# Performance work log

Hardware: AMD Instinct MI355X
Metric: run time of the kernel (lower is better)

Reference implementation:

```python
import jax, jax.numpy as jnp
import numpy as np

N_ENT = 14951   # entities (FB15K-style multimodal KG)
N_REL = 1345    # relations == number of context sub-graphs
N_NODES = 120000  # nodes in the batched context graph (b_x length)
N_EDGES = 480000  # edges in the normalized batched adjacency


def _glorot(key, shape):
    scale = np.sqrt(2.0 / (shape[0] + shape[1])).astype(np.float32)
    return jax.random.normal(key, shape, dtype=jnp.float32) * scale


def setup_inputs() -> dict:
    key = jax.random.key(0)
    ks = jax.random.split(key, 16)
    inp = {}
    inp["img_feat"] = jax.random.normal(ks[0], (N_ENT, 4096), dtype=jnp.float32)
    inp["text_feat"] = jax.random.normal(ks[1], (N_ENT, 300), dtype=jnp.float32)
    inp["rel_emb"] = jax.random.normal(ks[2], (N_REL, 300), dtype=jnp.float32)
    # learned parameters (eval mode: dropout = identity)
    inp["W_img_text"] = _glorot(ks[3], (4396, 100)); inp["b_img_text"] = jnp.zeros((100,), jnp.float32)
    inp["W_rel_input"] = _glorot(ks[4], (300, 100)); inp["b_rel_input"] = jnp.zeros((100,), jnp.float32)
    inp["W_gc1"] = _glorot(ks[5], (200, 256)); inp["b_gc1"] = jnp.zeros((256,), jnp.float32)
    inp["W_gc2"] = _glorot(ks[6], (256, 200)); inp["b_gc2"] = jnp.zeros((200,), jnp.float32)
    inp["W_emb"] = _glorot(ks[7], (400, 1)); inp["b_emb"] = jnp.zeros((1,), jnp.float32)
    inp["W_emb_out"] = _glorot(ks[8], (400, 200)); inp["b_emb_out"] = jnp.zeros((200,), jnp.float32)
    inp["W_rel"] = _glorot(ks[9], (300, 200)); inp["b_rel"] = jnp.zeros((200,), jnp.float32)
    # row-normalized adjacency of the batched context graph, as edge list
    inp["edge_weight"] = jax.random.uniform(ks[10], (N_EDGES,), dtype=jnp.float32)
    inp["b_x"] = jax.random.randint(ks[11], (N_NODES,), 0, N_ENT)
    inp["b_graph"] = jax.random.randint(ks[12], (N_NODES,), 0, N_REL)
    inp["edge_src"] = jax.random.randint(ks[13], (N_EDGES,), 0, N_NODES)
    inp["edge_dst"] = jax.random.randint(ks[14], (N_EDGES,), 0, N_NODES)
    return inp


def reference(img_feat, text_feat, rel_emb, W_img_text, b_img_text, W_rel_input,
              b_rel_input, W_gc1, b_gc1, W_gc2, b_gc2, W_emb, b_emb, W_emb_out,
              b_emb_out, W_rel, b_rel, edge_weight, b_x, b_graph, edge_src, edge_dst):
    seg_sum = lambda v, idx, n: jax.ops.segment_sum(v, idx, num_segments=n)

    def spmm(h):  # normalized adjacency @ h via edge-list gather/scatter
        return seg_sum(h[edge_src] * edge_weight[:, None], edge_dst, N_NODES)

    # multimodal entity encoder: Linear(4396 -> 100)
    emf = jnp.concatenate([img_feat, text_feat], axis=1) @ W_img_text + b_img_text
    # relation context encoder: Linear(300 -> 100) + ReLU
    rel_in = jax.nn.relu(rel_emb @ W_rel_input + b_rel_input)
    # batched context-graph node features [M, 200]
    h = jnp.concatenate([emf[b_x], rel_in[b_graph]], axis=1)
    # two-layer GCN encoder (SGCN1)
    h1 = jax.nn.relu(spmm(h @ W_gc1) + b_gc1)
    h2 = spmm(h1 @ W_gc2) + b_gc2          # [M, 200]
    # scatter_mean over entity ids, broadcast back
    cnt = seg_sum(jnp.ones((N_NODES,), h2.dtype), b_x, N_ENT)
    mean = seg_sum(h2, b_x, N_ENT) / jnp.maximum(cnt, 1.0)[:, None]
    emb = jnp.concatenate([h2, mean[b_x]], axis=1)   # [M, 400]
    score = emb @ W_emb + b_emb                      # [M, 1]
    # scatter_softmax over segments b_x (numerically stable)
    smax = jax.ops.segment_max(score, b_x, num_segments=N_ENT)
    e = jnp.exp(score - smax[b_x])
    z_s = e / seg_sum(e, b_x, N_ENT)[b_x]
    new_out = seg_sum(z_s * emb, b_x, N_ENT) @ W_emb_out + b_emb_out  # [N_ENT, 200]
    # relation output encoder: Linear(300 -> 200) + ReLU
    rel_context = jax.nn.relu(rel_emb @ W_rel + b_rel)                # [N_REL, 200]
    return new_out, rel_context
```

## Files before the change

### kernel.cpp

```cpp
#include <hip/hip_runtime.h>

#define N_ENT 14951
#define N_REL 1345
#define NNODE 120000
#define NEDGE 480000
#define MP_ENC 14976
#define KP_ENC 4480
#define NP_ENC 112
#define ENC_SPLIT 4
#define ENC_KSPLIT 1120
#define ENC_STEPS 35
#define MROWS1 16320
#define NB_E 118
#define NB_N 15

static inline int ceil_div(int a, int b){ return (a + b - 1) / b; }

typedef __bf16 bf16x8 __attribute__((ext_vector_type(8)));
typedef float f32x4 __attribute__((ext_vector_type(4)));

__device__ inline unsigned short f2bf(float f){
  unsigned u = __float_as_uint(f);
  return (unsigned short)((u + 0x7fffu + ((u >> 16) & 1u)) >> 16);
}
__device__ inline float bf2f(unsigned short b){
  return __uint_as_float(((unsigned)b) << 16);
}

__global__ __launch_bounds__(256) void enc_mfma(
    const float* __restrict__ img, const float* __restrict__ txt,
    const unsigned short* __restrict__ Wt1, float* __restrict__ part)
{
  __shared__ unsigned short As[64 * 40];
  __shared__ unsigned short Bs[112 * 40];
  const int t = threadIdx.x;
  const int m0 = blockIdx.x * 64;
  const int s = blockIdx.y;
  const int l = t & 63, w = t >> 6;
  f32x4 acc[7];
  #pragma unroll
  for (int i = 0; i < 7; i++) acc[i] = f32x4{0.f, 0.f, 0.f, 0.f};

  for (int step = 0; step < ENC_STEPS; ++step) {
    const int kb = s * ENC_KSPLIT + step * 32;
    #pragma unroll
    for (int p = 0; p < 2; ++p) {
      const int c = t + p * 256;
      const int row = c >> 3, kq = c & 7;
      const int rowg = m0 + row;
      const int k = kb + kq * 4;
      float4 v = make_float4(0.f, 0.f, 0.f, 0.f);
      if (rowg < N_ENT) {
        if (k < 4096)      v = *(const float4*)(img + (size_t)rowg * 4096 + k);
        else if (k < 4396) v = *(const float4*)(txt + (size_t)rowg * 300 + (k - 4096));
      }
      ushort4 b;
      b.x = f2bf(v.x); b.y = f2bf(v.y); b.z = f2bf(v.z); b.w = f2bf(v.w);
      *(ushort4*)&As[row * 40 + kq * 4] = b;
    }
    {
      const int n = t >> 2, k16 = t & 3;
      *(uint4*)&Bs[n * 40 + k16 * 8] = *(const uint4*)(Wt1 + (size_t)n * KP_ENC + kb + k16 * 8);
      if (t < 192) {
        const int c = t + 256;
        const int n2 = c >> 2, k2 = c & 3;
        *(uint4*)&Bs[n2 * 40 + k2 * 8] = *(const uint4*)(Wt1 + (size_t)n2 * KP_ENC + kb + k2 * 8);
      }
    }
    __syncthreads();
    bf16x8 a = *(const bf16x8*)&As[(w * 16 + (l & 15)) * 40 + (l >> 4) * 8];
    #pragma unroll
    for (int ct = 0; ct < 7; ++ct) {
      bf16x8 bb = *(const bf16x8*)&Bs[(ct * 16 + (l & 15)) * 40 + (l >> 4) * 8];
      acc[ct] = __builtin_amdgcn_mfma_f32_16x16x32_bf16(a, bb, acc[ct], 0, 0, 0);
    }
    __syncthreads();
  }
  const int rb = m0 + w * 16 + (l >> 4) * 4;
  const int col = l & 15;
  float* pp = part + (size_t)s * MP_ENC * NP_ENC;
  #pragma unroll
  for (int ct = 0; ct < 7; ++ct)
    #pragma unroll
    for (int i = 0; i < 4; ++i)
      pp[(size_t)(rb + i) * NP_ENC + ct * 16 + col] = acc[ct][i];
}

__global__ __launch_bounds__(256) void enc_reduce(
    const float* __restrict__ part, const float* __restrict__ bias,
    unsigned short* __restrict__ feat1)
{
  int i = blockIdx.x * 256 + threadIdx.x;
  if (i >= N_ENT * 100) return;
  int r = i / 100, c = i % 100;
  float v = bias[c];
  #pragma unroll
  for (int s = 0; s < ENC_SPLIT; ++s) v += part[((size_t)s * MP_ENC + r) * NP_ENC + c];
  feat1[(size_t)r * 224 + c] = f2bf(v);
}

__global__ __launch_bounds__(256) void rel_enc(
    const float* __restrict__ rel, const float* __restrict__ W_ri,
    const float* __restrict__ b_ri, unsigned short* __restrict__ feat1)
{
  __shared__ float rs[300];
  const int r = blockIdx.x;
  const int t = threadIdx.x;
  if (t < 75) {
    float4 v = *(const float4*)(rel + (size_t)r * 300 + t * 4);
    *(float4*)&rs[t * 4] = v;
  }
  __syncthreads();
  if (t >= 100) return;
  float s = b_ri[t];
  for (int k = 0; k < 300; ++k) s = fmaf(rs[k], W_ri[(size_t)k * 100 + t], s);
  feat1[(size_t)(N_ENT + r) * 224 + 100 + t] = f2bf(fmaxf(s, 0.f));
}

__global__ __launch_bounds__(256) void egr1_mfma(
    const unsigned short* __restrict__ feat1, const unsigned short* __restrict__ Wtg1,
    unsigned short* __restrict__ egr1)
{
  __shared__ unsigned short As[64 * 40];
  __shared__ unsigned short Bs[256 * 40];
  const int t = threadIdx.x;
  const int m0 = blockIdx.x * 64;
  const int l = t & 63, w = t >> 6;
  f32x4 acc[16];
  #pragma unroll
  for (int i = 0; i < 16; i++) acc[i] = f32x4{0.f, 0.f, 0.f, 0.f};

  for (int step = 0; step < 7; ++step) {
    const int kb = step * 32;
    {
      const int row = t >> 2, kc = t & 3;
      *(uint4*)&As[row * 40 + kc * 8] = *(const uint4*)(feat1 + (size_t)(m0 + row) * 224 + kb + kc * 8);
    }
    #pragma unroll
    for (int p = 0; p < 4; ++p) {
      const int c = t + p * 256;
      const int n = c >> 2, k16 = c & 3;
      *(uint4*)&Bs[n * 40 + k16 * 8] = *(const uint4*)(Wtg1 + (size_t)n * 224 + kb + k16 * 8);
    }
    __syncthreads();
    bf16x8 a = *(const bf16x8*)&As[(w * 16 + (l & 15)) * 40 + (l >> 4) * 8];
    #pragma unroll
    for (int ct = 0; ct < 16; ++ct) {
      bf16x8 bb = *(const bf16x8*)&Bs[(ct * 16 + (l & 15)) * 40 + (l >> 4) * 8];
      acc[ct] = __builtin_amdgcn_mfma_f32_16x16x32_bf16(a, bb, acc[ct], 0, 0, 0);
    }
    __syncthreads();
  }
  const int rb = m0 + w * 16 + (l >> 4) * 4;
  const int col0 = l & 15;
  #pragma unroll
  for (int ct = 0; ct < 16; ++ct) {
    const int col = ct * 16 + col0;
    #pragma unroll
    for (int i = 0; i < 4; ++i)
      egr1[(size_t)(rb + i) * 256 + col] = f2bf(acc[ct][i]);
  }
}

__global__ __launch_bounds__(256) void gemm2_mfma(
    const unsigned short* __restrict__ h1, const unsigned short* __restrict__ Wt2,
    unsigned short* __restrict__ hg2)
{
  __shared__ unsigned short As[64 * 40];
  __shared__ unsigned short Bs[208 * 40];
  const int t = threadIdx.x;
  const int m0 = blockIdx.x * 64;
  const int l = t & 63, w = t >> 6;
  f32x4 acc[13];
  #pragma unroll
  for (int i = 0; i < 13; i++) acc[i] = f32x4{0.f, 0.f, 0.f, 0.f};

  for (int step = 0; step < 8; ++step) {
    const int kb = step * 32;
    {
      const int row = t >> 2, kc = t & 3;
      *(uint4*)&As[row * 40 + kc * 8] = *(const uint4*)(h1 + (size_t)(m0 + row) * 256 + kb + kc * 8);
    }
    #pragma unroll
    for (int p = 0; p < 4; ++p) {
      const int c = t + p * 256;
      if (c < 832) {
        const int n = c >> 2, k16 = c & 3;
        *(uint4*)&Bs[n * 40 + k16 * 8] = *(const uint4*)(Wt2 + (size_t)n * 256 + kb + k16 * 8);
      }
    }
    __syncthreads();
    bf16x8 a = *(const bf16x8*)&As[(w * 16 + (l & 15)) * 40 + (l >> 4) * 8];
    #pragma unroll
    for (int ct = 0; ct < 13; ++ct) {
      bf16x8 bb = *(const bf16x8*)&Bs[(ct * 16 + (l & 15)) * 40 + (l >> 4) * 8];
      acc[ct] = __builtin_amdgcn_mfma_f32_16x16x32_bf16(a, bb, acc[ct], 0, 0, 0);
    }
    __syncthreads();
  }
  const int rb = m0 + w * 16 + (l >> 4) * 4;
  const int col0 = l & 15;
  #pragma unroll
  for (int ct = 0; ct < 13; ++ct) {
    const int col = ct * 16 + col0;
    #pragma unroll
    for (int i = 0; i < 4; ++i)
      hg2[(size_t)(rb + i) * 208 + col] = f2bf(acc[ct][i]);
  }
}

__global__ __launch_bounds__(256) void fin_mfma(
    const unsigned short* __restrict__ embA, const unsigned short* __restrict__ Wteo,
    const float* __restrict__ b_eo, float* __restrict__ out)
{
  __shared__ unsigned short As[64 * 40];
  __shared__ unsigned short Bs[208 * 40];
  const int t = threadIdx.x;
  const int m0 = blockIdx.x * 64;
  const int l = t & 63, w = t >> 6;
  f32x4 acc[13];
  #pragma unroll
  for (int i = 0; i < 13; i++) acc[i] = f32x4{0.f, 0.f, 0.f, 0.f};

  for (int step = 0; step < 13; ++step) {
    const int kb = step * 32;
    {
      const int row = t >> 2, kc = t & 3;
      *(uint4*)&As[row * 40 + kc * 8] = *(const uint4*)(embA + (size_t)(m0 + row) * 416 + kb + kc * 8);
    }
    #pragma unroll
    for (int p = 0; p < 4; ++p) {
      const int c = t + p * 256;
      if (c < 832) {
        const int n = c >> 2, k16 = c & 3;
        *(uint4*)&Bs[n * 40 + k16 * 8] = *(const uint4*)(Wteo + (size_t)n * 416 + kb + k16 * 8);
      }
    }
    __syncthreads();
    bf16x8 a = *(const bf16x8*)&As[(w * 16 + (l & 15)) * 40 + (l >> 4) * 8];
    #pragma unroll
    for (int ct = 0; ct < 13; ++ct) {
      bf16x8 bb = *(const bf16x8*)&Bs[(ct * 16 + (l & 15)) * 40 + (l >> 4) * 8];
      acc[ct] = __builtin_amdgcn_mfma_f32_16x16x32_bf16(a, bb, acc[ct], 0, 0, 0);
    }
    __syncthreads();
  }
  const int rb = m0 + w * 16 + (l >> 4) * 4;
  const int col0 = l & 15;
  #pragma unroll
  for (int ct = 0; ct < 13; ++ct) {
    const int col = ct * 16 + col0;
    if (col < 200) {
      const float b = b_eo[col];
      #pragma unroll
      for (int i = 0; i < 4; ++i) {
        const int r = rb + i;
        if (r < N_ENT) out[(size_t)r * 200 + col] = acc[ct][i] + b;
      }
    }
  }
}

__global__ __launch_bounds__(256) void wt_all_k(
    const float* __restrict__ W_it, const float* __restrict__ W_g1,
    const float* __restrict__ W_g2, const float* __restrict__ W_eo,
    unsigned short* __restrict__ Wt1, unsigned short* __restrict__ Wtg1,
    unsigned short* __restrict__ Wt2, unsigned short* __restrict__ Wteo)
{
  int i = blockIdx.x * 256 + threadIdx.x;
  if (i < NP_ENC * KP_ENC) {
    int n = i / KP_ENC, k = i % KP_ENC;
    float v = (n < 100 && k < 4396) ? W_it[(size_t)k * 100 + n] : 0.f;
    Wt1[i] = f2bf(v);
    return;
  }
  i -= NP_ENC * KP_ENC;
  if (i < 256 * 224) {
    int n = i / 224, k = i % 224;
    float v = (k < 200) ? W_g1[(size_t)k * 256 + n] : 0.f;
    Wtg1[i] = f2bf(v);
    return;
  }
  i -= 256 * 224;
  if (i < 208 * 256) {
    int n = i >> 8, k = i & 255;
    float v = (n < 200) ? W_g2[(size_t)k * 200 + n] : 0.f;
    Wt2[i] = f2bf(v);
    return;
  }
  i -= 208 * 256;
  if (i < 208 * 416) {
    int n = i / 416, k = i % 416;
    float v = (n < 200 && k < 400) ? W_eo[(size_t)k * 200 + n] : 0.f;
    Wteo[i] = f2bf(v);
  }
}

template<bool RELU, bool HASBIAS>
__global__ __launch_bounds__(256) void gemm_f32(
    const float* __restrict__ A1, int K1, const float* __restrict__ A2,
    const float* __restrict__ B, const float* __restrict__ bias,
    float* __restrict__ C, int M, int K, int N)
{
  constexpr int BM = 64, BN = 128, BK = 16;
  __shared__ float As[BK][BM + 4];
  __shared__ float Bs[BK][BN];
  const int t = threadIdx.x;
  const int m0 = blockIdx.y * BM, n0 = blockIdx.x * BN;
  const int tr = t >> 4, tc = t & 15;
  const int tm0 = tr * 4, tn0 = tc * 8;
  const int K2 = K - K1;
  const int arow = t >> 2, aq = (t & 3) * 4;
  const int brow = t >> 4, bc0 = (t & 15) * 4;
  float acc[4][8];
  #pragma unroll
  for (int i = 0; i < 4; i++)
    #pragma unroll
    for (int j = 0; j < 8; j++) acc[i][j] = 0.f;

  for (int k0 = 0; k0 < K; k0 += BK) {
    {
      const int r = m0 + arow;
      const int k = k0 + aq;
      float4 v = make_float4(0.f, 0.f, 0.f, 0.f);
      if (r < M) {
        if (k + 3 < K1) {
          v = *(const float4*)(A1 + (size_t)r * K1 + k);
        } else if (k >= K1 && (k - K1) + 3 < K2) {
          v = *(const float4*)(A2 + (size_t)r * K2 + (k - K1));
        } else {
          float tmp[4] = {0.f, 0.f, 0.f, 0.f};
          #pragma unroll
          for (int j = 0; j < 4; j++) {
            int kj = k + j;
            if (kj < K) tmp[j] = (kj < K1) ? A1[(size_t)r * K1 + kj]
                                           : A2[(size_t)r * K2 + (kj - K1)];
          }
          v = make_float4(tmp[0], tmp[1], tmp[2], tmp[3]);
        }
      }
      As[aq + 0][arow] = v.x; As[aq + 1][arow] = v.y;
      As[aq + 2][arow] = v.z; As[aq + 3][arow] = v.w;
    }
    {
      const int k = k0 + brow;
      #pragma unroll
      for (int h = 0; h < 2; h++) {
        const int n = n0 + bc0 + h * 64;
        float4 v = make_float4(0.f, 0.f, 0.f, 0.f);
        if (k < K) {
          if (n + 3 < N) {
            v = *(const float4*)(B + (size_t)k * N + n);
          } else {
            float tmp[4] = {0.f, 0.f, 0.f, 0.f};
            for (int j = 0; j < 4; j++) if (n + j < N) tmp[j] = B[(size_t)k * N + n + j];
            v = make_float4(tmp[0], tmp[1], tmp[2], tmp[3]);
          }
        }
        *(float4*)&Bs[brow][bc0 + h * 64] = v;
      }
    }
    __syncthreads();
    #pragma unroll
    for (int k = 0; k < BK; k++) {
      float a[4], b[8];
      *(float4*)&a[0] = *(const float4*)&As[k][tm0];
      *(float4*)&b[0] = *(const float4*)&Bs[k][tn0];
      *(float4*)&b[4] = *(const float4*)&Bs[k][tn0 + 4];
      #pragma unroll
      for (int i = 0; i < 4; i++)
        #pragma unroll
        for (int j = 0; j < 8; j++) acc[i][j] = fmaf(a[i], b[j], acc[i][j]);
    }
    __syncthreads();
  }
  #pragma unroll
  for (int i = 0; i < 4; i++) {
    const int r = m0 + tm0 + i;
    if (r >= M) continue;
    #pragma unroll
    for (int j = 0; j < 8; j++) {
      const int c = n0 + tn0 + j;
      if (c >= N) continue;
      float v = acc[i][j];
      if (HASBIAS) v += bias[c];
      if (RELU) v = fmaxf(v, 0.f);
      C[(size_t)r * N + c] = v;
    }
  }
}

__global__ __launch_bounds__(256) void hist2_k(
    const int* __restrict__ edst, const int* __restrict__ bx,
    int* __restrict__ ehist, int* __restrict__ nhist)
{
  int i = blockIdx.x * 256 + threadIdx.x;
  if (i < NEDGE) { atomicAdd(&ehist[edst[i]], 1); return; }
  i -= NEDGE;
  if (i < NNODE) atomicAdd(&nhist[bx[i]], 1);
}

__global__ __launch_bounds__(256) void scan1_k(
    const int* __restrict__ ehist, int* __restrict__ ebase, int* __restrict__ epart,
    const int* __restrict__ nhist, int* __restrict__ nbase, int* __restrict__ npart)
{
  __shared__ int s[256];
  const int t = threadIdx.x;
  const bool eregion = blockIdx.x < NB_E;
  const int b = eregion ? blockIdx.x : blockIdx.x - NB_E;
  const int n = eregion ? NNODE : N_ENT;
  const int* hist = eregion ? ehist : nhist;
  int* base = eregion ? ebase : nbase;
  int* partial = eregion ? epart : npart;
  const int i0 = b * 1024 + t * 4;
  int v[4];
  #pragma unroll
  for (int j = 0; j < 4; j++) v[j] = (i0 + j < n) ? hist[i0 + j] : 0;
  const int tsum = v[0] + v[1] + v[2] + v[3];
  s[t] = tsum;
  __syncthreads();
  #pragma unroll
  for (int off = 1; off < 256; off <<= 1) {
    int u = (t >= off) ? s[t - off] : 0;
    __syncthreads();
    s[t] += u;
    __syncthreads();
  }
  int run = s[t] - tsum;
  #pragma unroll
  for (int j = 0; j < 4; j++) {
    if (i0 + j < n) base[i0 + j] = run;
    run += v[j];
  }
  if (t == 255) partial[b] = s[255];
}

__global__ __launch_bounds__(256) void scan2_k(
    int* __restrict__ epart, int* __restrict__ ebase_end,
    int* __restrict__ npart, int* __restrict__ nbase_end)
{
  __shared__ int s[256];
  const int t = threadIdx.x;
  const bool eregion = blockIdx.x == 0;
  int* partial = eregion ? epart : npart;
  const int nb = eregion ? NB_E : NB_N;
  const int v = (t < nb) ? partial[t] : 0;
  s[t] = v;
  __syncthreads();
  #pragma unroll
  for (int off = 1; off < 256; off <<= 1) {
    int u = (t >= off) ? s[t - off] : 0;
    __syncthreads();
    s[t] += u;
    __syncthreads();
  }
  if (t < nb) partial[t] = s[t] - v;
  if (t == 255) *(eregion ? ebase_end : nbase_end) = s[255];
}

#define NB3_E 469
__global__ __launch_bounds__(256) void scan3_k(
    int* __restrict__ ebase, const int* __restrict__ epart,
    int* __restrict__ nbase, const int* __restrict__ npart)
{
  if (blockIdx.x < NB3_E) {
    int i = blockIdx.x * 256 + threadIdx.x;
    if (i < NNODE) ebase[i] += epart[i >> 10];
  } else {
    int i = (blockIdx.x - NB3_E) * 256 + threadIdx.x;
    if (i < N_ENT) nbase[i] += npart[i >> 10];
  }
}

__global__ __launch_bounds__(256) void scatter2_k(
    const int* __restrict__ esrc, const int* __restrict__ edst, const float* __restrict__ ew,
    const int* __restrict__ bx, const int* __restrict__ bg,
    const int* __restrict__ ebase, int* __restrict__ ecur,
    float* __restrict__ s_w, int* __restrict__ s_src,
    int* __restrict__ s_en, int* __restrict__ s_gn,
    const int* __restrict__ nbase, int* __restrict__ ncur, int* __restrict__ node_of)
{
  int i = blockIdx.x * 256 + threadIdx.x;
  if (i < NEDGE) {
    int d = edst[i];
    int p = ebase[d] + atomicAdd(&ecur[d], 1);
    int s = esrc[i];
    s_w[p] = ew[i];
    s_src[p] = s;
    s_en[p] = bx[s];
    s_gn[p] = bg[s];
    return;
  }
  i -= NEDGE;
  if (i < NNODE) {
    int ent = bx[i];
    int p = nbase[ent] + atomicAdd(&ncur[ent], 1);
    node_of[p] = i;
  }
}

__global__ __launch_bounds__(256) void spmm1_g(
    const int* __restrict__ ebase, const float* __restrict__ s_w,
    const int* __restrict__ s_en, const int* __restrict__ s_gn,
    const unsigned short* __restrict__ egr1,
    const float* __restrict__ b_g1, unsigned short* __restrict__ h1)
{
  const int gid = blockIdx.x * blockDim.x + threadIdx.x;
  const int d = gid >> 6, lane = gid & 63;
  if (d >= NNODE) return;
  const int p0 = ebase[d], p1 = ebase[d + 1];
  float acc[4] = {0.f, 0.f, 0.f, 0.f};
  for (int p = p0; p < p1; ++p) {
    const float w = s_w[p];
    const int en = s_en[p], gn = s_gn[p];
    const ushort4 va = *(const ushort4*)(egr1 + (size_t)en * 256 + lane * 4);
    const ushort4 vb = *(const ushort4*)(egr1 + (size_t)(N_ENT + gn) * 256 + lane * 4);
    acc[0] += w * (bf2f(va.x) + bf2f(vb.x));
    acc[1] += w * (bf2f(va.y) + bf2f(vb.y));
    acc[2] += w * (bf2f(va.z) + bf2f(vb.z));
    acc[3] += w * (bf2f(va.w) + bf2f(vb.w));
  }
  const float4 b = ((const float4*)b_g1)[lane];
  ushort4 o;
  o.x = f2bf(fmaxf(acc[0] + b.x, 0.f));
  o.y = f2bf(fmaxf(acc[1] + b.y, 0.f));
  o.z = f2bf(fmaxf(acc[2] + b.z, 0.f));
  o.w = f2bf(fmaxf(acc[3] + b.w, 0.f));
  *(ushort4*)(h1 + (size_t)d * 256 + lane * 4) = o;
}

__global__ __launch_bounds__(256) void spmm2_g(
    const int* __restrict__ ebase, const float* __restrict__ s_w,
    const int* __restrict__ s_src, const unsigned short* __restrict__ hg2,
    const float* __restrict__ b_g2, const float* __restrict__ W_e,
    unsigned short* __restrict__ h2, float* __restrict__ score)
{
  const int gid = blockIdx.x * blockDim.x + threadIdx.x;
  const int d = gid >> 6, lane = gid & 63;
  if (d >= NNODE) return;
  const int p0 = ebase[d], p1 = ebase[d + 1];
  float acc[4] = {0.f, 0.f, 0.f, 0.f};
  const int col = lane * 4;
  float sp = 0.f;
  if (lane < 50) {
    for (int p = p0; p < p1; ++p) {
      const float w = s_w[p];
      const ushort4 v = *(const ushort4*)(hg2 + (size_t)s_src[p] * 208 + col);
      acc[0] += w * bf2f(v.x); acc[1] += w * bf2f(v.y);
      acc[2] += w * bf2f(v.z); acc[3] += w * bf2f(v.w);
    }
    const float4 b = ((const float4*)b_g2)[lane];
    acc[0] += b.x; acc[1] += b.y; acc[2] += b.z; acc[3] += b.w;
    ushort4 o;
    o.x = f2bf(acc[0]); o.y = f2bf(acc[1]); o.z = f2bf(acc[2]); o.w = f2bf(acc[3]);
    *(ushort4*)(h2 + (size_t)d * 200 + col) = o;
    const float4 we = ((const float4*)W_e)[lane];
    sp = acc[0] * we.x + acc[1] * we.y + acc[2] * we.z + acc[3] * we.w;
  }
  #pragma unroll
  for (int off = 32; off; off >>= 1) sp += __shfl_xor(sp, off);
  if (lane == 0) score[d] = sp;
}

__global__ __launch_bounds__(256) void ent_k(
    const int* __restrict__ nbase, const int* __restrict__ node_of,
    const unsigned short* __restrict__ h2, const float* __restrict__ score,
    unsigned short* __restrict__ embA)
{
  const int gid = blockIdx.x * blockDim.x + threadIdx.x;
  const int ent = gid >> 6, lane = gid & 63;
  if (ent >= N_ENT) return;
  const int p0 = nbase[ent], p1 = nbase[ent + 1];
  const int cnt = p1 - p0;
  float m, es;
  if (cnt <= 64) {
    float sc = -3.4e38f;
    if (p0 + lane < p1) sc = score[node_of[p0 + lane]];
    m = sc;
    #pragma unroll
    for (int off = 32; off; off >>= 1) m = fmaxf(m, __shfl_xor(m, off));
    es = (p0 + lane < p1) ? __expf(sc - m) : 0.f;
    #pragma unroll
    for (int off = 32; off; off >>= 1) es += __shfl_xor(es, off);
  } else {
    m = -3.4e38f;
    for (int p = p0 + lane; p < p1; p += 64) m = fmaxf(m, score[node_of[p]]);
    #pragma unroll
    for (int off = 32; off; off >>= 1) m = fmaxf(m, __shfl_xor(m, off));
    es = 0.f;
    for (int p = p0 + lane; p < p1; p += 64) es += __expf(score[node_of[p]] - m);
    #pragma unroll
    for (int off = 32; off; off >>= 1) es += __shfl_xor(es, off);
  }
  const float inv_es = (cnt > 0) ? 1.f / es : 0.f;
  const float inv_cnt = 1.f / fmaxf((float)cnt, 1.f);
  float aw[4] = {0.f, 0.f, 0.f, 0.f};
  float am[4] = {0.f, 0.f, 0.f, 0.f};
  for (int p = p0; p < p1; ++p) {
    const int nd = node_of[p];
    const float z = __expf(score[nd] - m) * inv_es;
    if (lane < 50) {
      const ushort4 v = *(const ushort4*)(h2 + (size_t)nd * 200 + lane * 4);
      const float vx = bf2f(v.x), vy = bf2f(v.y), vz = bf2f(v.z), vw = bf2f(v.w);
      aw[0] += z * vx; aw[1] += z * vy; aw[2] += z * vz; aw[3] += z * vw;
      am[0] += vx; am[1] += vy; am[2] += vz; am[3] += vw;
    }
  }
  if (lane < 50) {
    ushort4 ow, om;
    ow.x = f2bf(aw[0]); ow.y = f2bf(aw[1]); ow.z = f2bf(aw[2]); ow.w = f2bf(aw[3]);
    om.x = f2bf(am[0] * inv_cnt); om.y = f2bf(am[1] * inv_cnt);
    om.z = f2bf(am[2] * inv_cnt); om.w = f2bf(am[3] * inv_cnt);
    *(ushort4*)(embA + (size_t)ent * 416 + lane * 4) = ow;
    *(ushort4*)(embA + (size_t)ent * 416 + 200 + lane * 4) = om;
  }
}

extern "C" void kernel_launch(void* const* d_in, const int* in_sizes, int n_in,
                              void* d_out, int out_size, void* d_ws, size_t ws_size,
                              hipStream_t stream)
{
  const float* img  = (const float*)d_in[0];
  const float* txt  = (const float*)d_in[1];
  const float* rel  = (const float*)d_in[2];
  const float* W_it = (const float*)d_in[3];
  const float* b_it = (const float*)d_in[4];
  const float* W_ri = (const float*)d_in[5];
  const float* b_ri = (const float*)d_in[6];
  const float* W_g1 = (const float*)d_in[7];
  const float* b_g1 = (const float*)d_in[8];
  const float* W_g2 = (const float*)d_in[9];
  const float* b_g2 = (const float*)d_in[10];
  const float* W_e  = (const float*)d_in[11];
  const float* W_eo = (const float*)d_in[13];
  const float* b_eo = (const float*)d_in[14];
  const float* W_r  = (const float*)d_in[15];
  const float* b_r  = (const float*)d_in[16];
  const float* ew   = (const float*)d_in[17];
  const int*   bx   = (const int*)d_in[18];
  const int*   bg   = (const int*)d_in[19];
  const int*   esrc = (const int*)d_in[20];
  const int*   edst = (const int*)d_in[21];

  float* ws = (float*)d_ws;
  size_t off = 0;
  auto alloc = [&](size_t n){ size_t r = off; off += (n + 255) & ~(size_t)255; return r; };
  unsigned short* feat1 = (unsigned short*)(ws + alloc((size_t)MROWS1 * 224 / 2));
  unsigned short* egr1  = (unsigned short*)(ws + alloc((size_t)MROWS1 * 256 / 2));
  unsigned short* h1    = (unsigned short*)(ws + alloc((size_t)NNODE * 256 / 2));
  unsigned short* hg2   = (unsigned short*)(ws + alloc((size_t)NNODE * 208 / 2));
  unsigned short* embA  = (unsigned short*)(ws + alloc((size_t)MP_ENC * 416 / 2));
  unsigned short* h2    = (unsigned short*)(ws + alloc((size_t)NNODE * 200 / 2));
  float* part  = ws + alloc((size_t)ENC_SPLIT * MP_ENC * NP_ENC);
  float* score = ws + alloc(NNODE);
  size_t cnt0 = alloc((size_t)NNODE * 2 + (size_t)N_ENT * 2);
  int* ehist = (int*)(ws + cnt0);
  int* ecur  = ehist + NNODE;
  int* nhist = ecur + NNODE;
  int* ncur  = nhist + N_ENT;
  int* ebase = (int*)(ws + alloc(NNODE + 1));
  int* nbase = (int*)(ws + alloc(N_ENT + 1));
  int* epart = (int*)(ws + alloc(256));
  int* npart = (int*)(ws + alloc(256));
  float* s_w  = ws + alloc(NEDGE);
  int* s_src  = (int*)(ws + alloc(NEDGE));
  int* s_en   = (int*)(ws + alloc(NEDGE));
  int* s_gn   = (int*)(ws + alloc(NEDGE));
  int* node_of = (int*)(ws + alloc(NNODE));
  unsigned short* Wt1  = (unsigned short*)(ws + alloc((size_t)NP_ENC * KP_ENC / 2));
  unsigned short* Wtg1 = (unsigned short*)(ws + alloc((size_t)256 * 224 / 2));
  unsigned short* Wt2  = (unsigned short*)(ws + alloc((size_t)208 * 256 / 2));
  unsigned short* Wteo = (unsigned short*)(ws + alloc((size_t)208 * 416 / 2));

  dim3 blk(256);

  hipMemsetAsync(ehist, 0, ((size_t)NNODE * 2 + (size_t)N_ENT * 2) * 4, stream);
  hipMemsetAsync(feat1, 0, (size_t)MROWS1 * 224 * 2, stream);
  hipMemsetAsync(embA,  0, (size_t)MP_ENC * 416 * 2, stream);

  hist2_k<<<ceil_div(NEDGE + NNODE, 256), blk, 0, stream>>>(edst, bx, ehist, nhist);
  scan1_k<<<NB_E + NB_N, blk, 0, stream>>>(ehist, ebase, epart, nhist, nbase, npart);
  scan2_k<<<2, blk, 0, stream>>>(epart, ebase + NNODE, npart, nbase + N_ENT);
  scan3_k<<<NB3_E + ceil_div(N_ENT, 256), blk, 0, stream>>>(ebase, epart, nbase, npart);
  scatter2_k<<<ceil_div(NEDGE + NNODE, 256), blk, 0, stream>>>(
      esrc, edst, ew, bx, bg, ebase, ecur, s_w, s_src, s_en, s_gn, nbase, ncur, node_of);

  wt_all_k<<<ceil_div(NP_ENC * KP_ENC + 256 * 224 + 208 * 256 + 208 * 416, 256), blk, 0, stream>>>(
      W_it, W_g1, W_g2, W_eo, Wt1, Wtg1, Wt2, Wteo);

  enc_mfma<<<dim3(MP_ENC / 64, ENC_SPLIT), blk, 0, stream>>>(img, txt, Wt1, part);
  enc_reduce<<<ceil_div(N_ENT * 100, 256), blk, 0, stream>>>(part, b_it, feat1);
  rel_enc<<<N_REL, blk, 0, stream>>>(rel, W_ri, b_ri, feat1);

  egr1_mfma<<<MROWS1 / 64, blk, 0, stream>>>(feat1, Wtg1, egr1);
  spmm1_g<<<ceil_div(NNODE * 64, 256), blk, 0, stream>>>(
      ebase, s_w, s_en, s_gn, egr1, b_g1, h1);

  gemm2_mfma<<<NNODE / 64, blk, 0, stream>>>(h1, Wt2, hg2);
  spmm2_g<<<ceil_div(NNODE * 64, 256), blk, 0, stream>>>(
      ebase, s_w, s_src, hg2, b_g2, W_e, h2, score);

  ent_k<<<ceil_div(N_ENT * 64, 256), blk, 0, stream>>>(nbase, node_of, h2, score, embA);

  float* out_new = (float*)d_out;
  float* out_rel = out_new + (size_t)N_ENT * 200;
  fin_mfma<<<MP_ENC / 64, blk, 0, stream>>>(embA, Wteo, b_eo, out_new);
  gemm_f32<true, true><<<dim3(2, ceil_div(N_REL, 64)), blk, 0, stream>>>(
      rel, 300, rel, W_r, b_r, out_rel, N_REL, 300, 200);
}
```

Before: 567.8 us.

## Widen encoder GEMM K-tile, raise split-K to 14, and reorder grid

The image/text encoder GEMM now stages a 64-wide K slice per step instead of 32, which halves the number of barrier pairs per unit of work. Split-K rises from 4 to 14 partitions, so far more blocks are available to fill the GPU. The grid is transposed so that neighbouring blocks cover different K ranges of the same 64 rows. The trade-off is a much larger partial-sum buffer that must be written and then read back by the reduction kernel, and it relies on that buffer and enc_reduce being sized from ENC_SPLIT.

```diff
diff --git a/kernel.cpp b/kernel.cpp
--- a/kernel.cpp
+++ b/kernel.cpp
@@ -7,9 +7,9 @@
 #define MP_ENC 14976
 #define KP_ENC 4480
 #define NP_ENC 112
-#define ENC_SPLIT 4
-#define ENC_KSPLIT 1120
-#define ENC_STEPS 35
+#define ENC_SPLIT 14
+#define ENC_KSPLIT 320
+#define ENC_STEPS 5
 #define MROWS1 16320
 #define NB_E 118
 #define NB_N 15
@@ -31,48 +31,60 @@
     const float* __restrict__ img, const float* __restrict__ txt,
     const unsigned short* __restrict__ Wt1, float* __restrict__ part)
 {
-  __shared__ unsigned short As[64 * 40];
-  __shared__ unsigned short Bs[112 * 40];
+  __shared__ unsigned short As[64 * 72];
+  __shared__ unsigned short Bs[112 * 72];
   const int t = threadIdx.x;
-  const int m0 = blockIdx.x * 64;
-  const int s = blockIdx.y;
+  const int s = blockIdx.x;
+  const int m0 = blockIdx.y * 64;
   const int l = t & 63, w = t >> 6;
   f32x4 acc[7];
   #pragma unroll
   for (int i = 0; i < 7; i++) acc[i] = f32x4{0.f, 0.f, 0.f, 0.f};
 
   for (int step = 0; step < ENC_STEPS; ++step) {
-    const int kb = s * ENC_KSPLIT + step * 32;
-    #pragma unroll
-    for (int p = 0; p < 2; ++p) {
-      const int c = t + p * 256;
-      const int row = c >> 3, kq = c & 7;
+    const int kb = s * ENC_KSPLIT + step * 64;
+    {
+      const int row = t >> 2;
+      const int q = (t & 3) * 16;
       const int rowg = m0 + row;
-      const int k = kb + kq * 4;
-      float4 v = make_float4(0.f, 0.f, 0.f, 0.f);
-      if (rowg < N_ENT) {
-        if (k < 4096)      v = *(const float4*)(img + (size_t)rowg * 4096 + k);
-        else if (k < 4396) v = *(const float4*)(txt + (size_t)rowg * 300 + (k - 4096));
+      const float* irow = img + (size_t)rowg * 4096;
+      const float* trow = txt + (size_t)rowg * 300;
+      ushort4 o[4];
+      #pragma unroll
+      for (int j = 0; j < 4; ++j) {
+        const int kj = kb + q + j * 4;
+        float4 v = make_float4(0.f, 0.f, 0.f, 0.f);
+        if (rowg < N_ENT) {
+          if (kj < 4096)       v = *(const float4*)(irow + kj);
+          else if (kj < 4396)  v = *(const float4*)(trow + (kj - 4096));
+        }
+        o[j].x = f2bf(v.x); o[j].y = f2bf(v.y); o[j].z = f2bf(v.z); o[j].w = f2bf(v.w);
       }
-      ushort4 b;
-      b.x = f2bf(v.x); b.y = f2bf(v.y); b.z = f2bf(v.z); b.w = f2bf(v.w);
-      *(ushort4*)&As[row * 40 + kq * 4] = b;
+      unsigned short* dst = &As[row * 72 + q];
+      *(ushort4*)(dst + 0)  = o[0];
+      *(ushort4*)(dst + 4)  = o[1];
+      *(ushort4*)(dst + 8)  = o[2];
+      *(ushort4*)(dst + 12) = o[3];
     }
     {
-      const int n = t >> 2, k16 = t & 3;
-      *(uint4*)&Bs[n * 40 + k16 * 8] = *(const uint4*)(Wt1 + (size_t)n * KP_ENC + kb + k16 * 8);
-      if (t < 192) {
-        const int c = t + 256;
-        const int n2 = c >> 2, k2 = c & 3;
-        *(uint4*)&Bs[n2 * 40 + k2 * 8] = *(const uint4*)(Wt1 + (size_t)n2 * KP_ENC + kb + k2 * 8);
+      #pragma unroll
+      for (int p = 0; p < 4; ++p) {
+        const int c = t + p * 256;
+        if (c < 896) {
+          const int n = c >> 3, ch = c & 7;
+          *(uint4*)&Bs[n * 72 + ch * 8] = *(const uint4*)(Wt1 + (size_t)n * KP_ENC + kb + ch * 8);
+        }
       }
     }
     __syncthreads();
-    bf16x8 a = *(const bf16x8*)&As[(w * 16 + (l & 15)) * 40 + (l >> 4) * 8];
-    #pragma unroll
-    for (int ct = 0; ct < 7; ++ct) {
-      bf16x8 bb = *(const bf16x8*)&Bs[(ct * 16 + (l & 15)) * 40 + (l >> 4) * 8];
-      acc[ct] = __builtin_amdgcn_mfma_f32_16x16x32_bf16(a, bb, acc[ct], 0, 0, 0);
+    #pragma unroll
+    for (int kh = 0; kh < 2; ++kh) {
+      bf16x8 a = *(const bf16x8*)&As[(w * 16 + (l & 15)) * 72 + kh * 32 + (l >> 4) * 8];
+      #pragma unroll
+      for (int ct = 0; ct < 7; ++ct) {
+        bf16x8 bb = *(const bf16x8*)&Bs[(ct * 16 + (l & 15)) * 72 + kh * 32 + (l >> 4) * 8];
+        acc[ct] = __builtin_amdgcn_mfma_f32_16x16x32_bf16(a, bb, acc[ct], 0, 0, 0);
+      }
     }
     __syncthreads();
   }
@@ -688,7 +700,7 @@
   wt_all_k<<<ceil_div(NP_ENC * KP_ENC + 256 * 224 + 208 * 256 + 208 * 416, 256), blk, 0, stream>>>(
       W_it, W_g1, W_g2, W_eo, Wt1, Wtg1, Wt2, Wteo);
 
-  enc_mfma<<<dim3(MP_ENC / 64, ENC_SPLIT), blk, 0, stream>>>(img, txt, Wt1, part);
+  enc_mfma<<<dim3(ENC_SPLIT, MP_ENC / 64), blk, 0, stream>>>(img, txt, Wt1, part);
   enc_reduce<<<ceil_div(N_ENT * 100, 256), blk, 0, stream>>>(part, b_it, feat1);
   rel_enc<<<N_REL, blk, 0, stream>>>(rel, W_ri, b_ri, feat1);
 
```

After: 624.8 us. 1.1x slower.
